# Optimization experiments

Hardware: AMD Instinct MI355X
Metric: run time of the kernel (lower is better)

The kernel has to match this reference:

```python
import jax, jax.numpy as jnp
import numpy as np

B, T, C, H = 2, 2048, 1024, 16
D = C // H  # head_dim = 64

def setup_inputs() -> dict:
    key = jax.random.key(0)
    k0, k1, k2, k3, k4 = jax.random.split(key, 5)
    s = 1.0 / np.sqrt(C)
    return {
        "x": jax.random.normal(k0, (B, T, C), dtype=jnp.float32),
        "w_qkv": jax.random.uniform(k1, (C, 3 * C), jnp.float32, -s, s),
        "b_qkv": jax.random.uniform(k2, (3 * C,), jnp.float32, -s, s),
        "w_proj": jax.random.uniform(k3, (C, C), jnp.float32, -s, s),
        "b_proj": jax.random.uniform(k4, (C,), jnp.float32, -s, s),
    }

def reference(x, w_qkv, b_qkv, w_proj, b_proj):
    Bx, Tx, Cx = x.shape
    qkv = x @ w_qkv + b_qkv                      # [B,T,3C]
    q, k, v = jnp.split(qkv, 3, axis=-1)
    # [B,T,C] -> [B,H,T,D]
    def heads(t):
        return t.reshape(Bx, Tx, H, D).transpose(0, 2, 1, 3)
    q, k, v = heads(q), heads(k), heads(v)
    att = jnp.einsum('bhqd,bhkd->bhqk', q, k) / np.sqrt(D).astype(np.float32)
    causal = jnp.tril(jnp.ones((Tx, Tx), dtype=bool))
    att = jnp.where(causal, att, -jnp.inf)
    att = jax.nn.softmax(att, axis=-1)
    y = jnp.einsum('bhqk,bhkd->bhqd', att, v)    # [B,H,T,D]
    y = y.transpose(0, 2, 1, 3).reshape(Bx, Tx, Cx)
    return y @ w_proj + b_proj
```

## Files before the change

kernel.cpp:

```cpp
#include <hip/hip_runtime.h>
#include <hip/hip_bf16.h>

typedef short bf16x8 __attribute__((ext_vector_type(8)));
typedef float f32x4 __attribute__((ext_vector_type(4)));
typedef unsigned short u16;
typedef unsigned short u16x8 __attribute__((ext_vector_type(8)));
typedef float f32x4_a __attribute__((ext_vector_type(4), may_alias));

__device__ __forceinline__ u16 f2bf(float f) {
    union { float f; unsigned u; } v; v.f = f;
    unsigned r = v.u + 0x7fffu + ((v.u >> 16) & 1u);
    return (u16)(r >> 16);
}
__device__ __forceinline__ unsigned pk2(float lo, float hi) {
    union { __hip_bfloat162 h; unsigned u; } v;
    v.h = __float22bfloat162_rn(make_float2(lo, hi));
    return v.u;
}

__device__ __forceinline__ void gld_lds16(const void* g, void* l) {
    __builtin_amdgcn_global_load_lds(
        (const __attribute__((address_space(1))) void*)g,
        (__attribute__((address_space(3))) void*)l, 16, 0, 0);
}

__global__ __launch_bounds__(256) void prep_kernel(
    const float* __restrict__ x, u16* __restrict__ xb,
    const float* __restrict__ w_qkv, u16* __restrict__ wqkvT) {
    __shared__ float tile[32][33];
    const int b = blockIdx.x, tid = threadIdx.x;
    if (b < 2048) {
        const int i = b * 256 + tid;
        float4 a = ((const float4*)x)[i * 2];
        float4 c = ((const float4*)x)[i * 2 + 1];
        u16x8 h;
        h[0] = f2bf(a.x); h[1] = f2bf(a.y); h[2] = f2bf(a.z); h[3] = f2bf(a.w);
        h[4] = f2bf(c.x); h[5] = f2bf(c.y); h[6] = f2bf(c.z); h[7] = f2bf(c.w);
        *(u16x8*)(xb + (size_t)i * 8) = h;
        return;
    }
    const int bx = b - 2048;
    const int n0 = (bx % 96) * 32, k0 = (bx / 96) * 32;
    const int tx = tid & 31, ty = tid >> 5;
#pragma unroll
    for (int i = 0; i < 32; i += 8)
        tile[ty + i][tx] = w_qkv[(size_t)(k0 + ty + i) * 3072 + n0 + tx];
    __syncthreads();
#pragma unroll
    for (int i = 0; i < 32; i += 8)
        wqkvT[(size_t)(n0 + ty + i) * 1024 + k0 + tx] = f2bf(tile[tx][ty + i]);
}

#define QSCALE 0.180336880f

__global__ __launch_bounds__(512, 2) void gemm_8ph(
    const u16* __restrict__ A, const u16* __restrict__ Bt,
    const float* __restrict__ bias,
    u16* __restrict__ Qo, u16* __restrict__ Ko, u16* __restrict__ Vt) {
    const int K = 1024;
    __shared__ __align__(16) u16 smem[40960];

    const int tid = threadIdx.x;
    const int lane = tid & 63, wid = tid >> 6;
    const int wm = wid >> 2, wn = wid & 3;
    const int fr = lane & 15, fq = lane >> 4;
    const int m0 = blockIdx.y * 128, n0 = blockIdx.x * 192;

    const int gsrc = (tid & 7) ^ ((tid >> 3) & 7);
    const u16* gA0 = A + (size_t)(m0 + (tid >> 3)) * K + gsrc * 8;
    const u16* gB0 = Bt + (size_t)(n0 + (tid >> 3)) * K + gsrc * 8;

    const int r7 = fr & 7;
    const int gk0 = ((0 + fq) ^ r7) * 8;
    const int gk1 = ((4 + fq) ^ r7) * 8;

    f32x4 acc[4][3];
#pragma unroll
    for (int m = 0; m < 4; m++)
#pragma unroll
        for (int n = 0; n < 3; n++)
#pragma unroll
            for (int r = 0; r < 4; r++) acc[m][n][r] = 0.f;

#define STAGE5(t)                                                               \
    do {                                                                        \
        const int _b = (t) & 1;                                                 \
        const size_t _ko = (size_t)(t) * 64;                                    \
        u16* _la = smem + _b * 8192 + wid * 512;                                \
        u16* _lb = smem + 16384 + _b * 12288 + wid * 512;                       \
        gld_lds16(gA0 + _ko, _la);                                              \
        gld_lds16(gA0 + (size_t)64 * 1024 + _ko, _la + 4096);                   \
        gld_lds16(gB0 + _ko, _lb);                                              \
        gld_lds16(gB0 + (size_t)64 * 1024 + _ko, _lb + 4096);                   \
        gld_lds16(gB0 + (size_t)128 * 1024 + _ko, _lb + 8192);                  \
    } while (0)

    STAGE5(0);
    asm volatile("s_waitcnt vmcnt(0)" ::: "memory");
    __builtin_amdgcn_s_barrier();

    for (int t = 0; t < 16; t++) {
        const int b = t & 1;
        const u16* lA = smem + b * 8192;
        const u16* lB = smem + 16384 + b * 12288;
        if (t + 1 < 16) STAGE5(t + 1);

        bf16x8 aR[4][2], b01[2][2], b2[2];

#pragma unroll
        for (int mf = 0; mf < 4; mf++) {
            const int row = (wm * 64 + mf * 16 + fr) * 64;
            aR[mf][0] = *(const bf16x8*)&lA[row + gk0];
            aR[mf][1] = *(const bf16x8*)&lA[row + gk1];
        }
#pragma unroll
        for (int nf = 0; nf < 2; nf++) {
            const int row = (wn * 48 + nf * 16 + fr) * 64;
            b01[nf][0] = *(const bf16x8*)&lB[row + gk0];
            b01[nf][1] = *(const bf16x8*)&lB[row + gk1];
        }
        __builtin_amdgcn_s_setprio(1);
#pragma unroll
        for (int mf = 0; mf < 4; mf++)
#pragma unroll
            for (int nf = 0; nf < 2; nf++) {
                acc[mf][nf] = __builtin_amdgcn_mfma_f32_16x16x32_bf16(aR[mf][0], b01[nf][0], acc[mf][nf], 0, 0, 0);
                acc[mf][nf] = __builtin_amdgcn_mfma_f32_16x16x32_bf16(aR[mf][1], b01[nf][1], acc[mf][nf], 0, 0, 0);
            }
        __builtin_amdgcn_s_setprio(0);
        __builtin_amdgcn_s_barrier();

        {
            const int row = (wn * 48 + 32 + fr) * 64;
            b2[0] = *(const bf16x8*)&lB[row + gk0];
            b2[1] = *(const bf16x8*)&lB[row + gk1];
        }
        __builtin_amdgcn_s_setprio(1);
#pragma unroll
        for (int mf = 0; mf < 4; mf++) {
            acc[mf][2] = __builtin_amdgcn_mfma_f32_16x16x32_bf16(aR[mf][0], b2[0], acc[mf][2], 0, 0, 0);
            acc[mf][2] = __builtin_amdgcn_mfma_f32_16x16x32_bf16(aR[mf][1], b2[1], acc[mf][2], 0, 0, 0);
        }
        __builtin_amdgcn_s_setprio(0);

        asm volatile("s_waitcnt vmcnt(0)" ::: "memory");
        __builtin_amdgcn_s_barrier();
    }
#undef STAGE5

#pragma unroll
    for (int mf = 0; mf < 4; mf++) {
#pragma unroll
        for (int nf = 0; nf < 3; nf++) {
            const int row0 = m0 + wm * 64 + mf * 16 + fq * 4;
            const int col = n0 + wn * 48 + nf * 16 + fr;
            float v4[4];
#pragma unroll
            for (int r = 0; r < 4; r++) v4[r] = acc[mf][nf][r] + bias[col];
            const int bb = row0 >> 11, t0 = row0 & 2047;
            const int sec = col >> 10, cc = col & 1023;
            const int h = cc >> 6, d = cc & 63;
            if (sec == 0) {
#pragma unroll
                for (int r = 0; r < 4; r++)
                    Qo[(((size_t)(bb * 16 + h) * 2048 + t0 + r) << 6) + d] = f2bf(v4[r] * QSCALE);
            } else if (sec == 1) {
#pragma unroll
                for (int r = 0; r < 4; r++)
                    Ko[(((size_t)(bb * 16 + h) * 2048 + t0 + r) << 6) + d] = f2bf(v4[r]);
            } else {
                ushort4 p;
                p.x = f2bf(v4[0]); p.y = f2bf(v4[1]); p.z = f2bf(v4[2]); p.w = f2bf(v4[3]);
                *(ushort4*)&Vt[(((size_t)(bb * 16 + h) * 64 + d) << 11) + t0] = p;
            }
        }
    }
}

template <int BN>
__global__ __launch_bounds__(256) void gemm_m97(
    const u16* __restrict__ A, const u16* __restrict__ Bt,
    const float* __restrict__ bias, float* __restrict__ Cf,
    int M, int N, int K) {
    constexpr int NF = BN / 32;
    __shared__ __align__(16) u16 lA[128 * 64];
    __shared__ __align__(16) u16 lB[BN * 64];

    const int tid = threadIdx.x;
    const int lane = tid & 63, wid = tid >> 6;
    const int wr = wid >> 1, wc = wid & 1;
    const int fr = lane & 15, fq = lane >> 4;
    const int m0 = blockIdx.y * 128, n0 = blockIdx.x * BN;

    const int gsrc = (lane & 7) ^ (lane >> 3);
    const u16* gA0 = A + (size_t)(m0 + (tid >> 3)) * K + gsrc * 8;
    const u16* gB0 = Bt + (size_t)(n0 + (tid >> 3)) * K + gsrc * 8;
    u16* lAw = lA + wid * 512;
    u16* lBw = lB + wid * 512;

    const int r7 = fr & 7;
    const int gk[2] = { ((0 + fq) ^ r7) * 8, ((4 + fq) ^ r7) * 8 };

    f32x4 acc[4][NF];
#pragma unroll
    for (int m = 0; m < 4; m++)
#pragma unroll
        for (int n = 0; n < NF; n++)
#pragma unroll
            for (int r = 0; r < 4; r++) acc[m][n][r] = 0.f;

    for (int k0 = 0; k0 < K; k0 += 64) {
        __syncthreads();
#pragma unroll
        for (int c = 0; c < 4; c++)
            gld_lds16(gA0 + (size_t)(c * 32) * K + k0, lAw + c * 2048);
#pragma unroll
        for (int c = 0; c < BN / 32; c++)
            gld_lds16(gB0 + (size_t)(c * 32) * K + k0, lBw + c * 2048);
        __syncthreads();

#pragma unroll
        for (int kf = 0; kf < 2; kf++) {
            bf16x8 a[4], b[NF];
#pragma unroll
            for (int m = 0; m < 4; m++)
                a[m] = *(const bf16x8*)&lA[(wr * 64 + m * 16 + fr) * 64 + gk[kf]];
#pragma unroll
            for (int n = 0; n < NF; n++)
                b[n] = *(const bf16x8*)&lB[(wc * (BN / 2) + n * 16 + fr) * 64 + gk[kf]];
#pragma unroll
            for (int m = 0; m < 4; m++)
#pragma unroll
                for (int n = 0; n < NF; n++)
                    acc[m][n] = __builtin_amdgcn_mfma_f32_16x16x32_bf16(a[m], b[n], acc[m][n], 0, 0, 0);
        }
    }

#pragma unroll
    for (int m = 0; m < 4; m++) {
#pragma unroll
        for (int n = 0; n < NF; n++) {
            const int row0 = m0 + wr * 64 + m * 16 + fq * 4;
            const int col = n0 + wc * (BN / 2) + n * 16 + fr;
#pragma unroll
            for (int r = 0; r < 4; r++)
                Cf[(size_t)(row0 + r) * N + col] = acc[m][n][r] + bias[col];
        }
    }
}

__global__ __launch_bounds__(256, 4) void attn_kernel(const u16* __restrict__ Q,
                                                      const u16* __restrict__ Kg,
                                                      const u16* __restrict__ Vt,
                                                      u16* __restrict__ O,
                                                      const float* __restrict__ wp,
                                                      u16* __restrict__ wpT) {
    __shared__ __align__(16) u16 smem[12288];

    const int tid = threadIdx.x;

    if (blockIdx.x >= 1024) {
        float* tile = (float*)smem;
        const int bx = blockIdx.x - 1024;
        const int n0 = (bx & 31) * 32, k0 = (bx >> 5) * 32;
        const int tx = tid & 31, ty = tid >> 5;
#pragma unroll
        for (int i = 0; i < 32; i += 8)
            tile[(ty + i) * 33 + tx] = wp[(size_t)(k0 + ty + i) * 1024 + n0 + tx];
        __syncthreads();
#pragma unroll
        for (int i = 0; i < 32; i += 8)
            wpT[(size_t)(n0 + ty + i) * 1024 + k0 + tx] = f2bf(tile[tx * 33 + ty + i]);
        return;
    }

    u16* lV = smem + 8192;
    const int lane = tid & 63, wid = tid >> 6;
    const int fr = lane & 15, fq = lane >> 4;
    const int kw = wid >> 1, qw = wid & 1;
    const int bh = blockIdx.x & 31;
    const int qi = 31 - (blockIdx.x >> 5);
    const int qb0 = qi * 64;
    const size_t base = (size_t)bh * (2048 * 64);
    const u16* Qp = Q + base;
    const u16* Kp = Kg + base;
    const u16* Vp = Vt + base;

    const int q0w = qb0 + qw * 32;
    bf16x8 qa[2][2];
#pragma unroll
    for (int qg = 0; qg < 2; qg++)
#pragma unroll
        for (int kf = 0; kf < 2; kf++)
            qa[qg][kf] = *(const bf16x8*)&Qp[(size_t)(q0w + qg * 16 + fr) * 64 + kf * 32 + fq * 8];

    bf16x8 vones;
#pragma unroll
    for (int j = 0; j < 8; j++) vones[j] = (short)0x3F80;

    f32x4 o[4][2], lsum[2];
#pragma unroll
    for (int qg = 0; qg < 2; qg++) {
#pragma unroll
        for (int r = 0; r < 4; r++) lsum[qg][r] = 0.f;
#pragma unroll
        for (int dg = 0; dg < 4; dg++)
#pragma unroll
            for (int r = 0; r < 4; r++) o[dg][qg][r] = 0.f;
    }

    const int srow0 = wid * 8 + (lane >> 3);
    const int gsrc = (lane & 7) ^ (lane >> 3);
    const u16* kSrc0 = Kp + (size_t)srow0 * 64 + gsrc * 8;
    const u16* vSrc0 = Vp + ((size_t)srow0 << 11) + gsrc * 8;

    const int r7 = fr & 7;
    const int gk0 = ((0 + fq) ^ r7) * 8;
    const int gk1 = ((4 + fq) ^ r7) * 8;
    const int gkv = ((kw * 4 + fq) ^ r7) * 8;

    const int nt = qi + 1;

#define STAGE_K(bufofs, kt0_)                                                   \
    do {                                                                        \
        u16* _lkw = smem + (bufofs) + wid * 512;                                \
        gld_lds16(kSrc0 + (size_t)(kt0_) * 64, _lkw);                           \
        gld_lds16(kSrc0 + (size_t)((kt0_) + 32) * 64, _lkw + 2048);             \
    } while (0)
#define STAGE_V(kt0_)                                                           \
    do {                                                                        \
        u16* _lvw = lV + wid * 512;                                             \
        gld_lds16(vSrc0 + (kt0_), _lvw);                                        \
        gld_lds16(vSrc0 + ((size_t)32 << 11) + (kt0_), _lvw + 2048);            \
    } while (0)

    STAGE_K(0, 0);
    STAGE_V(0);
    asm volatile("s_waitcnt vmcnt(0)" ::: "memory");
    __builtin_amdgcn_s_barrier();

    for (int kt = 0; kt < nt; kt++) {
        const int kt0 = kt << 6;
        const int curofs = (kt & 1) ? 4096 : 0;

        if (kt + 1 < nt) {
            STAGE_K(curofs ^ 4096, kt0 + 64);
            asm volatile("s_waitcnt vmcnt(2)" ::: "memory");
            __builtin_amdgcn_s_barrier();
        } else if (nt > 1) {
            asm volatile("s_waitcnt vmcnt(0)" ::: "memory");
            __builtin_amdgcn_s_barrier();
        }
        const u16* lKc = smem + curofs;

        f32x4 s[2][2];
#pragma unroll
        for (int kg = 0; kg < 2; kg++)
#pragma unroll
            for (int qg = 0; qg < 2; qg++)
#pragma unroll
                for (int r = 0; r < 4; r++) s[kg][qg][r] = 0.f;
        __builtin_amdgcn_s_setprio(1);
#pragma unroll
        for (int kg = 0; kg < 2; kg++) {
            const int krow = (kw * 32 + kg * 16 + fr) * 64;
            bf16x8 kb0 = *(const bf16x8*)&lKc[krow + gk0];
            bf16x8 kb1 = *(const bf16x8*)&lKc[krow + gk1];
#pragma unroll
            for (int qg = 0; qg < 2; qg++) {
                s[kg][qg] = __builtin_amdgcn_mfma_f32_16x16x32_bf16(kb0, qa[qg][0], s[kg][qg], 0, 0, 0);
                s[kg][qg] = __builtin_amdgcn_mfma_f32_16x16x32_bf16(kb1, qa[qg][1], s[kg][qg], 0, 0, 0);
            }
        }
        __builtin_amdgcn_s_setprio(0);

        if (kt == nt - 1) {
#pragma unroll
            for (int kg = 0; kg < 2; kg++) {
                const int kg0 = kt0 + kw * 32 + kg * 16 + fq * 4;
#pragma unroll
                for (int qg = 0; qg < 2; qg++) {
                    const int qg0 = q0w + qg * 16 + fr;
#pragma unroll
                    for (int r = 0; r < 4; r++)
                        if (kg0 + r > qg0) s[kg][qg][r] = -200.f;
                }
            }
        }

        bf16x8 va[4];
#pragma unroll
        for (int dg = 0; dg < 4; dg++)
            va[dg] = *(const bf16x8*)&lV[(dg * 16 + fr) * 64 + gkv];

#pragma unroll
        for (int qg = 0; qg < 2; qg++) {
            unsigned pa = pk2(__builtin_amdgcn_exp2f(s[0][qg][0]), __builtin_amdgcn_exp2f(s[0][qg][1]));
            unsigned pb_ = pk2(__builtin_amdgcn_exp2f(s[0][qg][2]), __builtin_amdgcn_exp2f(s[0][qg][3]));
            unsigned pc = pk2(__builtin_amdgcn_exp2f(s[1][qg][0]), __builtin_amdgcn_exp2f(s[1][qg][1]));
            unsigned pd = pk2(__builtin_amdgcn_exp2f(s[1][qg][2]), __builtin_amdgcn_exp2f(s[1][qg][3]));
            asm("v_permlane32_swap_b32 %0, %1" : "+v"(pa), "+v"(pc));
            asm("v_permlane16_swap_b32 %0, %1" : "+v"(pa), "+v"(pc));
            asm("v_permlane32_swap_b32 %0, %1" : "+v"(pb_), "+v"(pd));
            asm("v_permlane16_swap_b32 %0, %1" : "+v"(pb_), "+v"(pd));
            union { unsigned u[4]; bf16x8 v; } pbu;
            pbu.u[0] = pa; pbu.u[1] = pb_; pbu.u[2] = pc; pbu.u[3] = pd;
            const bf16x8 pb = pbu.v;

            __builtin_amdgcn_s_setprio(1);
            lsum[qg] = __builtin_amdgcn_mfma_f32_16x16x32_bf16(vones, pb, lsum[qg], 0, 0, 0);
#pragma unroll
            for (int dg = 0; dg < 4; dg++)
                o[dg][qg] = __builtin_amdgcn_mfma_f32_16x16x32_bf16(va[dg], pb, o[dg][qg], 0, 0, 0);
            __builtin_amdgcn_s_setprio(0);
        }

        if (kt + 1 < nt) {
            __builtin_amdgcn_s_barrier();
            STAGE_V(kt0 + 64);
        }
    }
#undef STAGE_K
#undef STAGE_V

    __syncthreads();

    float* cmb = (float*)smem;
    float* slab = cmb + (size_t)qw * 2560 + lane * 40;
    if (kw == 1) {
#pragma unroll
        for (int dg = 0; dg < 4; dg++)
#pragma unroll
            for (int qg = 0; qg < 2; qg++)
                *(f32x4_a*)&slab[(dg * 2 + qg) * 4] = o[dg][qg];
#pragma unroll
        for (int qg = 0; qg < 2; qg++)
            *(f32x4_a*)&slab[32 + qg * 4] = lsum[qg];
    }
    __syncthreads();
    if (kw == 0) {
#pragma unroll
        for (int dg = 0; dg < 4; dg++)
#pragma unroll
            for (int qg = 0; qg < 2; qg++) {
                f32x4_a p = *(const f32x4_a*)&slab[(dg * 2 + qg) * 4];
#pragma unroll
                for (int r = 0; r < 4; r++) o[dg][qg][r] += p[r];
            }
#pragma unroll
        for (int qg = 0; qg < 2; qg++) {
            f32x4_a p = *(const f32x4_a*)&slab[32 + qg * 4];
            lsum[qg][0] += p[0];
        }

        const int bb = bh >> 4, hh = bh & 15;
#pragma unroll
        for (int qg = 0; qg < 2; qg++) {
            const float inv = 1.f / lsum[qg][0];
            u16* orow = O + ((size_t)(bb * 2048 + q0w + qg * 16 + fr)) * 1024 + hh * 64 + fq * 4;
#pragma unroll
            for (int dg = 0; dg < 4; dg++) {
                ushort4 h;
                h.x = f2bf(o[dg][qg][0] * inv);
                h.y = f2bf(o[dg][qg][1] * inv);
                h.z = f2bf(o[dg][qg][2] * inv);
                h.w = f2bf(o[dg][qg][3] * inv);
                *(ushort4*)&orow[dg * 16] = h;
            }
        }
    }
}

extern "C" void kernel_launch(void* const* d_in, const int* in_sizes, int n_in,
                              void* d_out, int out_size, void* d_ws, size_t ws_size,
                              hipStream_t stream) {
    const float* x      = (const float*)d_in[0];
    const float* w_qkv  = (const float*)d_in[1];
    const float* b_qkv  = (const float*)d_in[2];
    const float* w_proj = (const float*)d_in[3];
    const float* b_proj = (const float*)d_in[4];
    float* out = (float*)d_out;

    u16* ws = (u16*)d_ws;
    u16* wqkvT  = ws;
    u16* wprojT = wqkvT + 3072 * 1024;
    u16* Qb     = wprojT + 1024 * 1024;
    u16* Kb     = Qb + 32 * 2048 * 64;
    u16* Vtb    = Kb + 32 * 2048 * 64;
    u16* xb     = Vtb + 32 * 2048 * 64;
    u16* attnO  = xb;

    prep_kernel<<<5120, 256, 0, stream>>>(x, xb, w_qkv, wqkvT);

    gemm_8ph<<<dim3(16, 32), 512, 0, stream>>>(xb, wqkvT, b_qkv, Qb, Kb, Vtb);

    attn_kernel<<<2048, 256, 0, stream>>>(Qb, Kb, Vtb, attnO, w_proj, wprojT);

    gemm_m97<64><<<dim3(16, 32), 256, 0, stream>>>(
        attnO, wprojT, b_proj, out, 4096, 1024, 1024);
}
```

Measured before the change: 90.83 us.

## Halve QKV GEMM waves per block and double each wave's output tile

Measured after the change: 90.83 us. No clear change (-0.0%).

```diff
diff --git a/kernel.cpp b/kernel.cpp
--- a/kernel.cpp
+++ b/kernel.cpp
@@ -53,7 +53,7 @@
 
 #define QSCALE 0.180336880f
 
-__global__ __launch_bounds__(512, 2) void gemm_8ph(
+__global__ __launch_bounds__(256, 2) void gemm_8ph(
     const u16* __restrict__ A, const u16* __restrict__ Bt,
     const float* __restrict__ bias,
     u16* __restrict__ Qo, u16* __restrict__ Ko, u16* __restrict__ Vt) {
@@ -62,7 +62,7 @@
 
     const int tid = threadIdx.x;
     const int lane = tid & 63, wid = tid >> 6;
-    const int wm = wid >> 2, wn = wid & 3;
+    const int wm = wid >> 1, wn = wid & 1;
     const int fr = lane & 15, fq = lane >> 4;
     const int m0 = blockIdx.y * 128, n0 = blockIdx.x * 192;
 
@@ -74,28 +74,33 @@
     const int gk0 = ((0 + fq) ^ r7) * 8;
     const int gk1 = ((4 + fq) ^ r7) * 8;
 
-    f32x4 acc[4][3];
+    f32x4 acc[4][6];
 #pragma unroll
     for (int m = 0; m < 4; m++)
 #pragma unroll
-        for (int n = 0; n < 3; n++)
+        for (int n = 0; n < 6; n++)
 #pragma unroll
             for (int r = 0; r < 4; r++) acc[m][n][r] = 0.f;
 
-#define STAGE5(t)                                                               \
+#define STAGE10(t)                                                              \
     do {                                                                        \
         const int _b = (t) & 1;                                                 \
         const size_t _ko = (size_t)(t) * 64;                                    \
         u16* _la = smem + _b * 8192 + wid * 512;                                \
         u16* _lb = smem + 16384 + _b * 12288 + wid * 512;                       \
         gld_lds16(gA0 + _ko, _la);                                              \
+        gld_lds16(gA0 + (size_t)32 * 1024 + _ko, _la + 2048);                   \
         gld_lds16(gA0 + (size_t)64 * 1024 + _ko, _la + 4096);                   \
+        gld_lds16(gA0 + (size_t)96 * 1024 + _ko, _la + 6144);                   \
         gld_lds16(gB0 + _ko, _lb);                                              \
+        gld_lds16(gB0 + (size_t)32 * 1024 + _ko, _lb + 2048);                   \
         gld_lds16(gB0 + (size_t)64 * 1024 + _ko, _lb + 4096);                   \
+        gld_lds16(gB0 + (size_t)96 * 1024 + _ko, _lb + 6144);                   \
         gld_lds16(gB0 + (size_t)128 * 1024 + _ko, _lb + 8192);                  \
+        gld_lds16(gB0 + (size_t)160 * 1024 + _ko, _lb + 10240);                 \
     } while (0)
 
-    STAGE5(0);
+    STAGE10(0);
     asm volatile("s_waitcnt vmcnt(0)" ::: "memory");
     __builtin_amdgcn_s_barrier();
 
@@ -103,9 +108,9 @@
         const int b = t & 1;
         const u16* lA = smem + b * 8192;
         const u16* lB = smem + 16384 + b * 12288;
-        if (t + 1 < 16) STAGE5(t + 1);
-
-        bf16x8 aR[4][2], b01[2][2], b2[2];
+        if (t + 1 < 16) STAGE10(t + 1);
+
+        bf16x8 aR[4][2], bR[3][2];
 
 #pragma unroll
         for (int mf = 0; mf < 4; mf++) {
@@ -114,46 +119,49 @@
             aR[mf][1] = *(const bf16x8*)&lA[row + gk1];
         }
 #pragma unroll
-        for (int nf = 0; nf < 2; nf++) {
-            const int row = (wn * 48 + nf * 16 + fr) * 64;
-            b01[nf][0] = *(const bf16x8*)&lB[row + gk0];
-            b01[nf][1] = *(const bf16x8*)&lB[row + gk1];
+        for (int nf = 0; nf < 3; nf++) {
+            const int row = (wn * 96 + nf * 16 + fr) * 64;
+            bR[nf][0] = *(const bf16x8*)&lB[row + gk0];
+            bR[nf][1] = *(const bf16x8*)&lB[row + gk1];
         }
         __builtin_amdgcn_s_setprio(1);
 #pragma unroll
         for (int mf = 0; mf < 4; mf++)
 #pragma unroll
-            for (int nf = 0; nf < 2; nf++) {
-                acc[mf][nf] = __builtin_amdgcn_mfma_f32_16x16x32_bf16(aR[mf][0], b01[nf][0], acc[mf][nf], 0, 0, 0);
-                acc[mf][nf] = __builtin_amdgcn_mfma_f32_16x16x32_bf16(aR[mf][1], b01[nf][1], acc[mf][nf], 0, 0, 0);
+            for (int nf = 0; nf < 3; nf++) {
+                acc[mf][nf] = __builtin_amdgcn_mfma_f32_16x16x32_bf16(aR[mf][0], bR[nf][0], acc[mf][nf], 0, 0, 0);
+                acc[mf][nf] = __builtin_amdgcn_mfma_f32_16x16x32_bf16(aR[mf][1], bR[nf][1], acc[mf][nf], 0, 0, 0);
             }
         __builtin_amdgcn_s_setprio(0);
         __builtin_amdgcn_s_barrier();
 
-        {
-            const int row = (wn * 48 + 32 + fr) * 64;
-            b2[0] = *(const bf16x8*)&lB[row + gk0];
-            b2[1] = *(const bf16x8*)&lB[row + gk1];
+#pragma unroll
+        for (int nf = 0; nf < 3; nf++) {
+            const int row = (wn * 96 + (nf + 3) * 16 + fr) * 64;
+            bR[nf][0] = *(const bf16x8*)&lB[row + gk0];
+            bR[nf][1] = *(const bf16x8*)&lB[row + gk1];
         }
         __builtin_amdgcn_s_setprio(1);
 #pragma unroll
-        for (int mf = 0; mf < 4; mf++) {
-            acc[mf][2] = __builtin_amdgcn_mfma_f32_16x16x32_bf16(aR[mf][0], b2[0], acc[mf][2], 0, 0, 0);
-            acc[mf][2] = __builtin_amdgcn_mfma_f32_16x16x32_bf16(aR[mf][1], b2[1], acc[mf][2], 0, 0, 0);
-        }
+        for (int mf = 0; mf < 4; mf++)
+#pragma unroll
+            for (int nf = 0; nf < 3; nf++) {
+                acc[mf][nf + 3] = __builtin_amdgcn_mfma_f32_16x16x32_bf16(aR[mf][0], bR[nf][0], acc[mf][nf + 3], 0, 0, 0);
+                acc[mf][nf + 3] = __builtin_amdgcn_mfma_f32_16x16x32_bf16(aR[mf][1], bR[nf][1], acc[mf][nf + 3], 0, 0, 0);
+            }
         __builtin_amdgcn_s_setprio(0);
 
         asm volatile("s_waitcnt vmcnt(0)" ::: "memory");
         __builtin_amdgcn_s_barrier();
     }
-#undef STAGE5
+#undef STAGE10
 
 #pragma unroll
     for (int mf = 0; mf < 4; mf++) {
 #pragma unroll
-        for (int nf = 0; nf < 3; nf++) {
+        for (int nf = 0; nf < 6; nf++) {
             const int row0 = m0 + wm * 64 + mf * 16 + fq * 4;
-            const int col = n0 + wn * 48 + nf * 16 + fr;
+            const int col = n0 + wn * 96 + nf * 16 + fr;
             float v4[4];
 #pragma unroll
             for (int r = 0; r < 4; r++) v4[r] = acc[mf][nf][r] + bias[col];
@@ -492,7 +500,7 @@
 
     prep_kernel<<<5120, 256, 0, stream>>>(x, xb, w_qkv, wqkvT);
 
-    gemm_8ph<<<dim3(16, 32), 512, 0, stream>>>(xb, wqkvT, b_qkv, Qb, Kb, Vtb);
+    gemm_8ph<<<dim3(16, 32), 256, 0, stream>>>(xb, wqkvT, b_qkv, Qb, Kb, Vtb);
 
     attn_kernel<<<2048, 256, 0, stream>>>(Qb, Kb, Vtb, attnO, w_proj, wprojT);
 
```
